# Kernel optimization log

Hardware: AMD Instinct MI355X
Metric: run time of the kernel (lower is better)

## Reference

```python
import jax, jax.numpy as jnp
import numpy as np

H = 16          # n_heads
EPS = 1e-3      # keras LayerNormalization default epsilon


def _layernorm(x, gamma, beta):
    m = jnp.mean(x, axis=-1, keepdims=True)
    v = jnp.var(x, axis=-1, keepdims=True)
    return (x - m) * jax.lax.rsqrt(v + EPS) * gamma + beta


def _mha(q, k, v, wq, bq, wk, bk, wv, bv, wo, bo, causal):
    B, Sq, D = q.shape
    Sk = k.shape[1]
    d = D // H
    qh = (q @ wq + bq).reshape(B, Sq, H, d)
    kh = (k @ wk + bk).reshape(B, Sk, H, d)
    vh = (v @ wv + bv).reshape(B, Sk, H, d)
    scores = jnp.einsum('bqhd,bkhd->bhqk', qh, kh) / jnp.sqrt(jnp.asarray(d, qh.dtype))
    if causal:
        mask = jnp.tril(jnp.ones((Sq, Sk), dtype=bool))
        scores = jnp.where(mask, scores, jnp.asarray(-1e9, scores.dtype))
    attn = jax.nn.softmax(scores, axis=-1)
    out = jnp.einsum('bhqk,bkhd->bqhd', attn, vh).reshape(B, Sq, D)
    return out @ wo + bo


def setup_inputs() -> dict:
    key = jax.random.key(0)
    B, S, D, DFF = 4, 1024, 1024, 4096
    ks = jax.random.split(key, 16)
    sc = 0.02
    inp = {
        'inputs': jax.random.normal(ks[0], (B, S, D), jnp.float32),
        'enc_outputs': jax.random.normal(ks[1], (B, S, D), jnp.float32),
    }
    # self-attention (mha1)
    inp['wq1'] = jax.random.normal(ks[2], (D, D), jnp.float32) * sc
    inp['wk1'] = jax.random.normal(ks[3], (D, D), jnp.float32) * sc
    inp['wv1'] = jax.random.normal(ks[4], (D, D), jnp.float32) * sc
    inp['wo1'] = jax.random.normal(ks[5], (D, D), jnp.float32) * sc
    inp['bq1'] = jnp.zeros((D,), jnp.float32)
    inp['bk1'] = jnp.zeros((D,), jnp.float32)
    inp['bv1'] = jnp.zeros((D,), jnp.float32)
    inp['bo1'] = jnp.zeros((D,), jnp.float32)
    # cross-attention (mha2)
    inp['wq2'] = jax.random.normal(ks[6], (D, D), jnp.float32) * sc
    inp['wk2'] = jax.random.normal(ks[7], (D, D), jnp.float32) * sc
    inp['wv2'] = jax.random.normal(ks[8], (D, D), jnp.float32) * sc
    inp['wo2'] = jax.random.normal(ks[9], (D, D), jnp.float32) * sc
    inp['bq2'] = jnp.zeros((D,), jnp.float32)
    inp['bk2'] = jnp.zeros((D,), jnp.float32)
    inp['bv2'] = jnp.zeros((D,), jnp.float32)
    inp['bo2'] = jnp.zeros((D,), jnp.float32)
    # FFN
    inp['w_ff1'] = jax.random.normal(ks[10], (D, DFF), jnp.float32) * sc
    inp['b_ff1'] = jnp.zeros((DFF,), jnp.float32)
    inp['w_ff2'] = jax.random.normal(ks[11], (DFF, D), jnp.float32) * sc
    inp['b_ff2'] = jnp.zeros((D,), jnp.float32)
    # LayerNorms
    for i in (1, 2, 3):
        inp[f'g{i}'] = jnp.ones((D,), jnp.float32)
        inp[f'be{i}'] = jnp.zeros((D,), jnp.float32)
    return inp


def reference(inputs, enc_outputs,
              wq1, bq1, wk1, bk1, wv1, bv1, wo1, bo1,
              wq2, bq2, wk2, bk2, wv2, bv2, wo2, bo2,
              w_ff1, b_ff1, w_ff2, b_ff2,
              g1, be1, g2, be2, g3, be3):
    # self-attention block (causal) + residual + LN; dropout is identity (eval)
    a1 = _mha(inputs, inputs, inputs, wq1, bq1, wk1, bk1, wv1, bv1, wo1, bo1, causal=True)
    o1 = _layernorm(inputs + a1, g1, be1)
    # cross-attention block + residual + LN
    a2 = _mha(o1, enc_outputs, enc_outputs, wq2, bq2, wk2, bk2, wv2, bv2, wo2, bo2, causal=False)
    o2 = _layernorm(o1 + a2, g2, be2)
    # FFN block + residual + LN
    f = jax.nn.relu(o2 @ w_ff1 + b_ff1) @ w_ff2 + b_ff2
    return _layernorm(o2 + f, g3, be3)
```

## Files before the change

### kernel.cpp

```cpp
#include <hip/hip_runtime.h>
#include <stdint.h>
#include <stddef.h>

typedef __attribute__((ext_vector_type(4))) float  floatx4;
typedef __attribute__((ext_vector_type(8))) short  short8;
typedef __attribute__((ext_vector_type(4))) short  short4v;

__device__ __forceinline__ float bf2f(short s) {
  union { uint32_t u; float f; } v;
  v.u = ((uint32_t)(uint16_t)s) << 16;
  return v.f;
}
__device__ __forceinline__ short f2bf(float f) {
  union { float f; uint32_t u; } v; v.f = f;
  uint32_t r = v.u + 0x7fffu + ((v.u >> 16) & 1u);
  return (short)(r >> 16);
}

__device__ __forceinline__ void async_cp16(const void* g, void* l) {
  __builtin_amdgcn_global_load_lds(
      (__attribute__((address_space(1))) void*)g,
      (__attribute__((address_space(3))) void*)l, 16, 0, 0);
}

__device__ __forceinline__ int swzb(int row, int bcol) {
  return ((row << 7) + bcol) ^ ((row & 7) << 4);
}

struct TransTable {
  const float* src[10];
  short*       dst[10];
  int K[10], N[10], base[10];
};
__global__ __launch_bounds__(256)
void transpose_all(TransTable tt)
{
  __shared__ short tile[32][33];
  int e = 0;
  #pragma unroll
  for (int i = 1; i < 10; i++) if ((int)blockIdx.x >= tt.base[i]) e = i;
  const int t = blockIdx.x - tt.base[e];
  const int N = tt.N[e], K = tt.K[e];
  const int ncols = N >> 5;
  const int n0 = (t % ncols) << 5, k0 = (t / ncols) << 5;
  const float* src = tt.src[e];
  short* dst = tt.dst[e];
  const int tx = threadIdx.x & 31, ty = threadIdx.x >> 5;
  #pragma unroll
  for (int i = 0; i < 32; i += 8)
    tile[ty + i][tx] = f2bf(src[(size_t)(k0 + ty + i) * N + n0 + tx]);
  __syncthreads();
  #pragma unroll
  for (int i = 0; i < 32; i += 8)
    dst[(size_t)(n0 + ty + i) * K + k0 + tx] = tile[tx][ty + i];
}

__global__ __launch_bounds__(256)
void convert_xe(const float* __restrict__ x, const float* __restrict__ enc,
                short* __restrict__ xc, short* __restrict__ encc)
{
  int b = blockIdx.x;
  const float* s; short* d;
  if (b < 4096) { s = x; d = xc; } else { s = enc; d = encc; b -= 4096; }
  const int i = (b * 256 + threadIdx.x) * 4;
  const floatx4 v = *(const floatx4*)(s + i);
  short4v o;
  #pragma unroll
  for (int j = 0; j < 4; j++) o[j] = f2bf(v[j]);
  *(short4v*)(d + i) = o;
}

struct ParamMap { const float* s[19]; int off[19]; };
__global__ __launch_bounds__(256)
void convert_params(ParamMap pm, short* __restrict__ dst)
{
  const int b = blockIdx.x;
  for (int t = threadIdx.x; t < 1024; t += 256)
    dst[b * 1024 + t] = f2bf(pm.s[b][pm.off[b] + t]);
}

template<int RELU, int RESID, int BM>
__global__ __launch_bounds__(256)
void gemm_bt(const short* __restrict__ A, const short* __restrict__ BT,
             const short* __restrict__ bias, const short* __restrict__ resid,
             short* __restrict__ C, int M, int N, int K)
{
  constexpr int MT = BM / 32;
  __shared__ short8 As[BM * 4];
  __shared__ short8 Bs[512];
  const int tid  = threadIdx.x;
  const int w    = tid >> 6;
  const int lane = tid & 63;
  const int m16  = lane & 15;
  const int g    = lane >> 4;
  const int nbn  = N >> 7;
  const int bid  = ((int)blockIdx.x & 7) * ((int)gridDim.x >> 3) + ((int)blockIdx.x >> 3);
  const int bm   = bid / nbn;
  const int bn   = bid % nbn;
  const int wm   = (w >> 1) * (BM / 2);
  const int wn   = (w & 1) << 6;

  const int r0 = lane >> 2;
  const int c0 = lane & 3;
  const short* pA = A  + (size_t)(bm * BM + w * (BM / 4) + r0) * K + c0 * 8;
  const short* pB = BT + (size_t)(bn * 128 + w * 32 + r0) * K + c0 * 8;
  short8* ldsA = As + w * BM;
  short8* ldsB = Bs + w * 128;

  floatx4 acc[MT][4];
  #pragma unroll
  for (int i = 0; i < MT; i++)
    #pragma unroll
    for (int j = 0; j < 4; j++)
      acc[i][j] = floatx4{0.f, 0.f, 0.f, 0.f};

  for (int k0 = 0; k0 < K; k0 += 32) {
    __syncthreads();
    async_cp16(pA + k0, ldsA);
    if (BM == 128) async_cp16(pA + k0 + 16 * (size_t)K, ldsA + 64);
    async_cp16(pB + k0,                  ldsB);
    async_cp16(pB + k0 + 16 * (size_t)K, ldsB + 64);
    __syncthreads();
    short8 af[MT], bfr[4];
    #pragma unroll
    for (int mt = 0; mt < MT; mt++)
      af[mt] = As[(wm + mt * 16 + m16) * 4 + g];
    #pragma unroll
    for (int nt = 0; nt < 4; nt++)
      bfr[nt] = Bs[(wn + nt * 16 + m16) * 4 + g];
    #pragma unroll
    for (int mt = 0; mt < MT; mt++)
      #pragma unroll
      for (int nt = 0; nt < 4; nt++)
        acc[mt][nt] = __builtin_amdgcn_mfma_f32_16x16x32_bf16(af[mt], bfr[nt], acc[mt][nt], 0, 0, 0);
  }

  #pragma unroll
  for (int mt = 0; mt < MT; mt++) {
    const int rbase = bm * BM + wm + mt * 16 + g * 4;
    #pragma unroll
    for (int nt = 0; nt < 4; nt++) {
      const int col = bn * 128 + wn + nt * 16 + m16;
      const float bia = bf2f(bias[col]);
      #pragma unroll
      for (int r = 0; r < 4; r++) {
        const size_t idx = (size_t)(rbase + r) * N + col;
        float v = acc[mt][nt][r] + bia;
        if (RESID) v += bf2f(resid[idx]);
        if (RELU)  v = fmaxf(v, 0.f);
        C[idx] = f2bf(v);
      }
    }
  }
}

template<int CAUSAL>
__global__ __launch_bounds__(256, 4)
void attention(const short* __restrict__ Qp, int ldq,
               const short* __restrict__ Kp, int ldk,
               const short* __restrict__ Vp, int ldv,
               short* __restrict__ Op, int ldo)
{
  const int S   = 1024;
  const int bid = blockIdx.x;
  const int qt  = bid & 15;
  const int h   = (bid >> 4) & 15;
  const int b   = bid >> 8;
  const int tid = threadIdx.x;
  const int w   = tid >> 6;
  const int lane = tid & 63;
  const int m16 = lane & 15;
  const int g   = lane >> 4;

  __shared__ __align__(16) short Ks[2][64 * 64];
  __shared__ __align__(16) short VT[2][64 * 64];
  __shared__ __align__(16) short Ps[4][16 * 64];

  const int rowQ = b * S + qt * 64;
  const int wrow = w * 16;

  const short* qsrc = Qp + (size_t)(rowQ + wrow + m16) * ldq + h * 64 + 8 * g;
  const short8 qf0 = *(const short8*)qsrc;
  const short8 qf1 = *(const short8*)(qsrc + 32);

  float mrow[4] = {-1e38f, -1e38f, -1e38f, -1e38f};
  float lrow[4] = {0.f, 0.f, 0.f, 0.f};
  floatx4 oacc[4];
  #pragma unroll
  for (int dt = 0; dt < 4; dt++) oacc[dt] = floatx4{0.f, 0.f, 0.f, 0.f};

  const int kr  = tid >> 2, kc = (tid & 3) << 4;
  const int vkp = (tid & 31) * 2, vcg = (tid >> 5) << 3;

  const short* kbase = Kp + (size_t)(b * S + kr)  * ldk + h * 64 + kc;
  const short* vbase = Vp + (size_t)(b * S + vkp) * ldv + h * 64 + vcg;

  const int nkt = CAUSAL ? (qt + 1) : (S / 64);

  short8 kst0 = *(const short8*)kbase;
  short8 kst1 = *(const short8*)(kbase + 8);
  short8 vst0 = *(const short8*)vbase;
  short8 vst1 = *(const short8*)(vbase + ldv);
  {
    char* kd = (char*)&Ks[0][0];
    *(short8*)(kd + swzb(kr, kc * 2))      = kst0;
    *(short8*)(kd + swzb(kr, kc * 2 + 16)) = kst1;
    char* vd = (char*)&VT[0][0];
    #pragma unroll
    for (int j = 0; j < 8; j++) {
      const uint32_t pk = (uint32_t)(uint16_t)vst0[j] | ((uint32_t)(uint16_t)vst1[j] << 16);
      *(uint32_t*)(vd + swzb(vcg + j, vkp * 2)) = pk;
    }
  }
  __syncthreads();

  for (int kt = 0; kt < nkt; kt++) {
    const int cur  = kt & 1;
    const int more = (kt + 1 < nkt);

    if (more) {
      const size_t roff = (size_t)(kt + 1) * 64;
      kst0 = *(const short8*)(kbase + roff * ldk);
      kst1 = *(const short8*)(kbase + roff * ldk + 8);
      vst0 = *(const short8*)(vbase + roff * ldv);
      vst1 = *(const short8*)(vbase + roff * ldv + ldv);
    }

    const int kb = kt * 64;

    const char* ksrc = (const char*)&Ks[cur][0];
    floatx4 sc[4];
    #pragma unroll
    for (int cg4 = 0; cg4 < 4; cg4++) {
      const short8 kfa = *(const short8*)(ksrc + swzb(cg4 * 16 + m16, 16 * g));
      const short8 kfb = *(const short8*)(ksrc + swzb(cg4 * 16 + m16, 64 + 16 * g));
      sc[cg4] = __builtin_amdgcn_mfma_f32_16x16x32_bf16(qf0, kfa, floatx4{0.f,0.f,0.f,0.f}, 0, 0, 0);
      sc[cg4] = __builtin_amdgcn_mfma_f32_16x16x32_bf16(qf1, kfb, sc[cg4], 0, 0, 0);
    }

    char* pbase = (char*)&Ps[w][0];
    #pragma unroll
    for (int r = 0; r < 4; r++) {
      float v0 = sc[0][r] * 0.125f, v1 = sc[1][r] * 0.125f;
      float v2 = sc[2][r] * 0.125f, v3 = sc[3][r] * 0.125f;
      if (CAUSAL && kt == qt) {
        const int qi = qt * 64 + wrow + g * 4 + r;
        if (kb + m16 > qi)      v0 = -1e9f;
        if (kb + 16 + m16 > qi) v1 = -1e9f;
        if (kb + 32 + m16 > qi) v2 = -1e9f;
        if (kb + 48 + m16 > qi) v3 = -1e9f;
      }
      float t = fmaxf(fmaxf(v0, v1), fmaxf(v2, v3));
      t = fmaxf(t, __shfl_xor(t, 1));
      t = fmaxf(t, __shfl_xor(t, 2));
      t = fmaxf(t, __shfl_xor(t, 4));
      t = fmaxf(t, __shfl_xor(t, 8));
      const float mn = fmaxf(mrow[r], t);
      const float alpha = __expf(mrow[r] - mn);
      mrow[r] = mn;
      v0 = __expf(v0 - mn); v1 = __expf(v1 - mn);
      v2 = __expf(v2 - mn); v3 = __expf(v3 - mn);
      float rs = (v0 + v1) + (v2 + v3);
      rs += __shfl_xor(rs, 1);
      rs += __shfl_xor(rs, 2);
      rs += __shfl_xor(rs, 4);
      rs += __shfl_xor(rs, 8);
      lrow[r] = lrow[r] * alpha + rs;
      #pragma unroll
      for (int dt = 0; dt < 4; dt++) oacc[dt][r] *= alpha;
      const int q = g * 4 + r;
      *(short*)(pbase + swzb(q, 2 * m16))      = f2bf(v0);
      *(short*)(pbase + swzb(q, 2 * m16 + 32)) = f2bf(v1);
      *(short*)(pbase + swzb(q, 2 * m16 + 64)) = f2bf(v2);
      *(short*)(pbase + swzb(q, 2 * m16 + 96)) = f2bf(v3);
    }

    asm volatile("s_waitcnt lgkmcnt(0)" ::: "memory");
    __builtin_amdgcn_sched_barrier(0);

    const short8 pf0 = *(const short8*)(pbase + swzb(m16, 16 * g));
    const short8 pf1 = *(const short8*)(pbase + swzb(m16, 64 + 16 * g));
    const char* vsrc = (const char*)&VT[cur][0];
    #pragma unroll
    for (int dt = 0; dt < 4; dt++) {
      const short8 vfa = *(const short8*)(vsrc + swzb(dt * 16 + m16, 16 * g));
      const short8 vfb = *(const short8*)(vsrc + swzb(dt * 16 + m16, 64 + 16 * g));
      oacc[dt] = __builtin_amdgcn_mfma_f32_16x16x32_bf16(pf0, vfa, oacc[dt], 0, 0, 0);
      oacc[dt] = __builtin_amdgcn_mfma_f32_16x16x32_bf16(pf1, vfb, oacc[dt], 0, 0, 0);
    }

    if (more) {
      char* kd = (char*)&Ks[cur ^ 1][0];
      *(short8*)(kd + swzb(kr, kc * 2))      = kst0;
      *(short8*)(kd + swzb(kr, kc * 2 + 16)) = kst1;
      char* vd = (char*)&VT[cur ^ 1][0];
      #pragma unroll
      for (int j = 0; j < 8; j++) {
        const uint32_t pk = (uint32_t)(uint16_t)vst0[j] | ((uint32_t)(uint16_t)vst1[j] << 16);
        *(uint32_t*)(vd + swzb(vcg + j, vkp * 2)) = pk;
      }
      __syncthreads();
    }
  }

  #pragma unroll
  for (int dt = 0; dt < 4; dt++)
    #pragma unroll
    for (int r = 0; r < 4; r++) {
      const size_t orow = (size_t)(rowQ + wrow + g * 4 + r);
      Op[orow * ldo + h * 64 + dt * 16 + m16] = f2bf(oacc[dt][r] / lrow[r]);
    }
}

template<int FINAL>
__global__ __launch_bounds__(256)
void layernorm_bf16(const short* __restrict__ x, const short* __restrict__ gamma,
                    const short* __restrict__ beta, void* __restrict__ out)
{
  const int D = 1024;
  const int row = blockIdx.x, tid = threadIdx.x;
  const short* xr = x + (size_t)row * D;
  short4v xv = *(const short4v*)(xr + tid * 4);
  float v[4], s = 0.f, ss = 0.f;
  #pragma unroll
  for (int j = 0; j < 4; j++) { v[j] = bf2f(xv[j]); s += v[j]; ss += v[j] * v[j]; }
  #pragma unroll
  for (int off = 32; off; off >>= 1) { s += __shfl_xor(s, off); ss += __shfl_xor(ss, off); }
  __shared__ float red[8];
  const int w = tid >> 6, lane = tid & 63;
  if (lane == 0) { red[w] = s; red[4 + w] = ss; }
  __syncthreads();
  s  = red[0] + red[1] + red[2] + red[3];
  ss = red[4] + red[5] + red[6] + red[7];
  const float mean = s * (1.f / D);
  const float var  = ss * (1.f / D) - mean * mean;
  const float inv  = rsqrtf(var + 1e-3f);
  float o[4];
  #pragma unroll
  for (int j = 0; j < 4; j++)
    o[j] = (v[j] - mean) * inv * bf2f(gamma[tid * 4 + j]) + bf2f(beta[tid * 4 + j]);
  if (FINAL) {
    floatx4 ov;
    #pragma unroll
    for (int j = 0; j < 4; j++) ov[j] = o[j];
    *(floatx4*)((float*)out + (size_t)row * D + tid * 4) = ov;
  } else {
    short4v ov;
    #pragma unroll
    for (int j = 0; j < 4; j++) ov[j] = f2bf(o[j]);
    *(short4v*)((short*)out + (size_t)row * D + tid * 4) = ov;
  }
}

extern "C" void kernel_launch(void* const* d_in, const int* in_sizes, int n_in,
                              void* d_out, int out_size, void* d_ws, size_t ws_size,
                              hipStream_t stream) {
  (void)in_sizes; (void)n_in; (void)out_size; (void)ws_size;
  const int M = 4096;
  const size_t MM = 1024 * 1024;

  short* ws = (short*)d_ws;
  short* wt_qkv1 = ws;
  short* wt_o1   = wt_qkv1 + 3 * MM;
  short* wt_q2   = wt_o1 + MM;
  short* wt_kv2  = wt_q2 + MM;
  short* wt_o2   = wt_kv2 + 2 * MM;
  short* wt_ff1  = wt_o2 + MM;
  short* wt_ff2  = wt_ff1 + 4 * MM;
  short* P       = ws + 16 * MM;
  short* encc    = ws + 16 * MM + 32768;
  short* act0    = encc + 4 * MM;
  short* attn    = act0 + 16 * MM;
  short* t1      = attn + 4 * MM;
  short* t2      = t1 + 4 * MM;
  short* xc      = t2;

  short* bqkv1 = P,        *bo1  = P + 3072, *bkv2 = P + 4096, *bq2 = P + 6144;
  short* bo2   = P + 7168, *bff1 = P + 8192, *bff2 = P + 12288;
  short* g1 = P + 13312, *be1 = P + 14336, *g2 = P + 15360, *be2 = P + 16384;
  short* g3 = P + 17408, *be3 = P + 18432;

  ParamMap pm;
  const int srcidx[19] = {6, 7, 8, 9, 15, 16, 14, 17, 19, 19, 19, 19, 21, 22, 23, 24, 25, 26, 27};
  const int offs[19]   = {0, 0, 0, 0, 0,  0,  0,  0,  0, 1024, 2048, 3072, 0, 0, 0, 0, 0, 0, 0};
  for (int i = 0; i < 19; i++) { pm.s[i] = (const float*)d_in[srcidx[i]]; pm.off[i] = offs[i]; }
  convert_params<<<19, 256, 0, stream>>>(pm, P);

  convert_xe<<<8192, 256, 0, stream>>>((const float*)d_in[0], (const float*)d_in[1], xc, encc);

  TransTable tt;
  const int widx[10] = {2, 3, 4, 5, 10, 11, 12, 13, 18, 20};
  short* wdst[10] = {wt_qkv1, wt_qkv1 + MM, wt_qkv1 + 2 * MM, wt_o1, wt_q2,
                     wt_kv2, wt_kv2 + MM, wt_o2, wt_ff1, wt_ff2};
  const int wK[10] = {1024, 1024, 1024, 1024, 1024, 1024, 1024, 1024, 1024, 4096};
  const int wN[10] = {1024, 1024, 1024, 1024, 1024, 1024, 1024, 1024, 4096, 1024};
  int base = 0;
  for (int i = 0; i < 10; i++) {
    tt.src[i] = (const float*)d_in[widx[i]];
    tt.dst[i] = wdst[i];
    tt.K[i] = wK[i]; tt.N[i] = wN[i]; tt.base[i] = base;
    base += (wN[i] / 32) * (wK[i] / 32);
  }
  transpose_all<<<base, 256, 0, stream>>>(tt);

  short* qkv1 = act0;
  gemm_bt<0, 0, 128><<<dim3((M / 128) * (3072 / 128)), 256, 0, stream>>>(
      xc, wt_qkv1, bqkv1, nullptr, qkv1, M, 3072, 1024);
  attention<1><<<dim3(1024), 256, 0, stream>>>(
      qkv1, 3072, qkv1 + 1024, 3072, qkv1 + 2048, 3072, attn, 1024);
  gemm_bt<0, 1, 64><<<dim3((M / 64) * (1024 / 128)), 256, 0, stream>>>(
      attn, wt_o1, bo1, xc, t1, M, 1024, 1024);
  layernorm_bf16<0><<<dim3(4096), 256, 0, stream>>>(t1, g1, be1, t1);

  short* kv2 = act0;
  short* q2  = act0 + 8 * MM;
  gemm_bt<0, 0, 128><<<dim3((M / 128) * (2048 / 128)), 256, 0, stream>>>(
      encc, wt_kv2, bkv2, nullptr, kv2, M, 2048, 1024);
  gemm_bt<0, 0, 64><<<dim3((M / 64) * (1024 / 128)), 256, 0, stream>>>(
      t1, wt_q2, bq2, nullptr, q2, M, 1024, 1024);
  attention<0><<<dim3(1024), 256, 0, stream>>>(
      q2, 1024, kv2, 2048, kv2 + 1024, 2048, attn, 1024);
  gemm_bt<0, 1, 64><<<dim3((M / 64) * (1024 / 128)), 256, 0, stream>>>(
      attn, wt_o2, bo2, t1, t2, M, 1024, 1024);
  layernorm_bf16<0><<<dim3(4096), 256, 0, stream>>>(t2, g2, be2, t2);

  short* hidden = act0;
  gemm_bt<1, 0, 128><<<dim3((M / 128) * (4096 / 128)), 256, 0, stream>>>(
      t2, wt_ff1, bff1, nullptr, hidden, M, 4096, 1024);
  gemm_bt<0, 1, 64><<<dim3((M / 64) * (1024 / 128)), 256, 0, stream>>>(
      hidden, wt_ff2, bff2, t2, attn, M, 1024, 4096);
  layernorm_bf16<1><<<dim3(4096), 256, 0, stream>>>(attn, g3, be3, d_out);
}
```

Measured before the change: 576.9 us.

## Double-buffer LDS tiles in bf16 GEMM to overlap loads with MFMA

The GEMM kernel now keeps two LDS buffers each for A and B. While one 32-wide K slice is being multiplied, the async global-to-LDS copies for the next slice are already in flight. The main loop advances 64 per iteration with one barrier per half-step instead of two per slice, which is meant to hide global load latency behind MFMA work. This doubles the kernel's shared-memory use, which may reduce occupancy, and it assumes K is a multiple of 64.

```diff
diff --git a/kernel.cpp b/kernel.cpp
--- a/kernel.cpp
+++ b/kernel.cpp
@@ -86,8 +86,10 @@
              short* __restrict__ C, int M, int N, int K)
 {
   constexpr int MT = BM / 32;
-  __shared__ short8 As[BM * 4];
-  __shared__ short8 Bs[512];
+  __shared__ short8 As0[BM * 4];
+  __shared__ short8 As1[BM * 4];
+  __shared__ short8 Bs0[512];
+  __shared__ short8 Bs1[512];
   const int tid  = threadIdx.x;
   const int w    = tid >> 6;
   const int lane = tid & 63;
@@ -104,8 +106,6 @@
   const int c0 = lane & 3;
   const short* pA = A  + (size_t)(bm * BM + w * (BM / 4) + r0) * K + c0 * 8;
   const short* pB = BT + (size_t)(bn * 128 + w * 32 + r0) * K + c0 * 8;
-  short8* ldsA = As + w * BM;
-  short8* ldsB = Bs + w * 128;
 
   floatx4 acc[MT][4];
   #pragma unroll
@@ -114,25 +114,38 @@
     for (int j = 0; j < 4; j++)
       acc[i][j] = floatx4{0.f, 0.f, 0.f, 0.f};
 
-  for (int k0 = 0; k0 < K; k0 += 32) {
-    __syncthreads();
-    async_cp16(pA + k0, ldsA);
-    if (BM == 128) async_cp16(pA + k0 + 16 * (size_t)K, ldsA + 64);
-    async_cp16(pB + k0,                  ldsB);
-    async_cp16(pB + k0 + 16 * (size_t)K, ldsB + 64);
-    __syncthreads();
+  auto stage = [&](short8* AS, short8* BS, int k0) {
+    async_cp16(pA + k0, AS + w * BM);
+    if constexpr (BM == 128) async_cp16(pA + k0 + 16 * (size_t)K, AS + w * BM + 64);
+    async_cp16(pB + k0,                  BS + w * 128);
+    async_cp16(pB + k0 + 16 * (size_t)K, BS + w * 128 + 64);
+  };
+  auto compute = [&](const short8* AS, const short8* BS) {
     short8 af[MT], bfr[4];
     #pragma unroll
     for (int mt = 0; mt < MT; mt++)
-      af[mt] = As[(wm + mt * 16 + m16) * 4 + g];
+      af[mt] = AS[(wm + mt * 16 + m16) * 4 + g];
     #pragma unroll
     for (int nt = 0; nt < 4; nt++)
-      bfr[nt] = Bs[(wn + nt * 16 + m16) * 4 + g];
+      bfr[nt] = BS[(wn + nt * 16 + m16) * 4 + g];
     #pragma unroll
     for (int mt = 0; mt < MT; mt++)
       #pragma unroll
       for (int nt = 0; nt < 4; nt++)
         acc[mt][nt] = __builtin_amdgcn_mfma_f32_16x16x32_bf16(af[mt], bfr[nt], acc[mt][nt], 0, 0, 0);
+  };
+
+  stage(As0, Bs0, 0);
+  __syncthreads();
+
+  for (int k0 = 0; k0 < K; k0 += 64) {
+    stage(As1, Bs1, k0 + 32);
+    compute(As0, Bs0);
+    __syncthreads();
+    if (k0 + 64 < K)
+      stage(As0, Bs0, k0 + 64);
+    compute(As1, Bs1);
+    __syncthreads();
   }
 
   #pragma unroll
```

After: 543.1 us. 5.9% less time.
